# Kernel optimization log

Hardware: AMD Instinct MI355X
Metric: run time of the kernel (lower is better)

The kernel has to match this reference:

```python
import jax, jax.numpy as jnp
import numpy as np

H = 4  # n_heads in nn.MultiheadAttention
LN_EPS = 1e-5


def _mha_seq1(x_q, x_kv, in_w, in_b, out_w, out_b):
    """torch nn.MultiheadAttention with batch_first and seq_len=1 on q and kv.
    x_q, x_kv: [B, F]. in_w: [3F, F] (packed q/k/v), out_w: [F, F].
    With a single kv position, softmax over the kv axis is identically 1,
    so the output equals out_proj(v); we still compute scores/softmax so the
    math (and zero grads to Wq/Wk) matches torch exactly.
    """
    B, F = x_q.shape
    dh = F // H
    wq, wk, wv = jnp.split(in_w, 3, axis=0)
    bq, bk, bv = jnp.split(in_b, 3, axis=0)
    q = (x_q @ wq.T + bq).reshape(B, H, dh)
    k = (x_kv @ wk.T + bk).reshape(B, H, dh)
    v = (x_kv @ wv.T + bv).reshape(B, H, dh)
    s = jnp.einsum('bhd,bhd->bh', q, k) / jnp.sqrt(jnp.asarray(dh, x_q.dtype))
    w = jax.nn.softmax(s[..., None], axis=-1)  # [B, H, 1] == 1
    o = (w * v).reshape(B, F)
    return o @ out_w.T + out_b


def _layer_norm(x, g, b):
    mu = jnp.mean(x, axis=-1, keepdims=True)
    var = jnp.mean(jnp.square(x - mu), axis=-1, keepdims=True)
    return (x - mu) * jax.lax.rsqrt(var + LN_EPS) * g + b


def setup_inputs() -> dict:
    key = jax.random.key(0)
    B, GD, TD, F = 16384, 1024, 1024, 2048
    ks = jax.random.split(key, 20)
    s = 0.02  # weight init scale
    return {
        'graph_feat': jax.random.normal(ks[0], (B, GD), jnp.float32),
        'temporal_feat': jax.random.normal(ks[1], (B, TD), jnp.float32),
        'gp_w': jax.random.normal(ks[2], (F, GD), jnp.float32) * s,
        'gp_b': jax.random.normal(ks[3], (F,), jnp.float32) * s,
        'tp_w': jax.random.normal(ks[4], (F, TD), jnp.float32) * s,
        'tp_b': jax.random.normal(ks[5], (F,), jnp.float32) * s,
        'in1_w': jax.random.normal(ks[6], (3 * F, F), jnp.float32) * s,
        'in1_b': jax.random.normal(ks[7], (3 * F,), jnp.float32) * s,
        'out1_w': jax.random.normal(ks[8], (F, F), jnp.float32) * s,
        'out1_b': jax.random.normal(ks[9], (F,), jnp.float32) * s,
        'in2_w': jax.random.normal(ks[10], (3 * F, F), jnp.float32) * s,
        'in2_b': jax.random.normal(ks[11], (3 * F,), jnp.float32) * s,
        'out2_w': jax.random.normal(ks[12], (F, F), jnp.float32) * s,
        'out2_b': jax.random.normal(ks[13], (F,), jnp.float32) * s,
        'gate_w': jax.random.normal(ks[14], (F, 2 * F), jnp.float32) * s,
        'gate_b': jax.random.normal(ks[15], (F,), jnp.float32) * s,
        'ln_g': jnp.ones((F,), jnp.float32),
        'ln_b': jnp.zeros((F,), jnp.float32),
        'lin_w': jax.random.normal(ks[16], (F, F), jnp.float32) * s,
        'lin_b': jax.random.normal(ks[17], (F,), jnp.float32) * s,
    }


def reference(graph_feat, temporal_feat, gp_w, gp_b, tp_w, tp_b,
              in1_w, in1_b, out1_w, out1_b, in2_w, in2_b, out2_w, out2_b,
              gate_w, gate_b, ln_g, ln_b, lin_w, lin_b):
    g = graph_feat @ gp_w.T + gp_b          # [B, F]
    t = temporal_feat @ tp_w.T + tp_b       # [B, F]
    attn1 = _mha_seq1(g, t, in1_w, in1_b, out1_w, out1_b)  # cross1(g, t, t)
    attn2 = _mha_seq1(t, g, in2_w, in2_b, out2_w, out2_b)  # cross2(t, g, g)
    cross = attn1 + attn2
    gate = jax.nn.sigmoid(jnp.concatenate([g, cross], axis=-1) @ gate_w.T + gate_b)
    fused = gate * g + (1.0 - gate) * cross
    fused = _layer_norm(fused + g, ln_g, ln_b)
    return fused @ lin_w.T + lin_b
```

## Files before the change

kernel.cpp:

```cpp
#include <hip/hip_runtime.h>
#include <stdint.h>

typedef __attribute__((ext_vector_type(8))) short short8;
typedef __attribute__((ext_vector_type(4))) float f32x4;

__device__ __forceinline__ unsigned short f2bf(float f) {
  union { float f; uint32_t u; } v; v.f = f;
  uint32_t u = v.u;
  u += 0x7FFF + ((u >> 16) & 1);
  return (unsigned short)(u >> 16);
}
__device__ __forceinline__ float bf2f(unsigned short h) {
  union { uint32_t u; float f; } v; v.u = ((uint32_t)h) << 16;
  return v.f;
}

__global__ void conv_kernel(const float* __restrict__ in,
                            unsigned short* __restrict__ out, int n) {
  long i = ((long)blockIdx.x * blockDim.x + threadIdx.x) * 8;
  if (i >= n) return;
  float4 a = *(const float4*)(in + i);
  float4 b = *(const float4*)(in + i + 4);
  short8 s;
  s[0] = (short)f2bf(a.x); s[1] = (short)f2bf(a.y);
  s[2] = (short)f2bf(a.z); s[3] = (short)f2bf(a.w);
  s[4] = (short)f2bf(b.x); s[5] = (short)f2bf(b.y);
  s[6] = (short)f2bf(b.z); s[7] = (short)f2bf(b.w);
  *(short8*)(out + i) = s;
}

__global__ void convcat_kernel(const float* __restrict__ in,
                               unsigned short* __restrict__ out,
                               int colbase, int n) {
  long i = ((long)blockIdx.x * blockDim.x + threadIdx.x) * 8;
  if (i >= n) return;
  float4 a = *(const float4*)(in + i);
  float4 b = *(const float4*)(in + i + 4);
  short8 s;
  s[0] = (short)f2bf(a.x); s[1] = (short)f2bf(a.y);
  s[2] = (short)f2bf(a.z); s[3] = (short)f2bf(a.w);
  s[4] = (short)f2bf(b.x); s[5] = (short)f2bf(b.y);
  s[6] = (short)f2bf(b.z); s[7] = (short)f2bf(b.w);
  long row = i >> 10, col = i & 1023;
  *(short8*)(out + row * 2048 + colbase + col) = s;
}

__global__ void convs_kernel(const float* __restrict__ in,
                             const float* __restrict__ scale,
                             unsigned short* __restrict__ out, int n) {
  long i = ((long)blockIdx.x * blockDim.x + threadIdx.x) * 8;
  if (i >= n) return;
  short8 s;
#pragma unroll
  for (int j = 0; j < 8; ++j)
    s[j] = (short)f2bf(in[i + j] * scale[(i + j) & 2047]);
  *(short8*)(out + i) = s;
}

__global__ void tconv_kernel(const float* __restrict__ in, int R, int C,
                             unsigned short* __restrict__ out) {
  __shared__ float tile[32][33];
  int c0 = blockIdx.x * 32, r0 = blockIdx.y * 32;
  int tx = threadIdx.x, ty = threadIdx.y;
#pragma unroll
  for (int i = 0; i < 32; i += 8)
    tile[ty + i][tx] = in[(long)(r0 + ty + i) * C + c0 + tx];
  __syncthreads();
#pragma unroll
  for (int i = 0; i < 32; i += 8)
    out[(long)(c0 + ty + i) * R + r0 + tx] = f2bf(tile[tx][ty + i]);
}

enum { CE_PLAIN = 0, CE_WT = 1, CE_ACC = 2 };

template <int CE>
__global__ __launch_bounds__(256)
void compose_kernel(const unsigned short* __restrict__ A, int lda,
                    const unsigned short* __restrict__ W, int ldw,
                    unsigned short* C, int ldc,
                    unsigned short* Ct, long ctoff,
                    int K, int nmt,
                    int pairBase, long aoff, long woff, long coff) {
  constexpr int BK = 32;
  __shared__ unsigned short sA[128 * BK];
  __shared__ unsigned short sB[128 * BK];
  const int tid  = threadIdx.x;
  const int lane = tid & 63;
  const int wave = tid >> 6;
  const int wr = (wave >> 1) * 64;
  const int wc = (wave & 1) * 64;

  int bid = blockIdx.x;
  if (bid >= pairBase) {
    bid -= pairBase;
    A += aoff; W += woff; C += coff; Ct += ctoff;
  }
  const long tileM = (long)(bid % nmt) * 128;
  const long tileN = (long)(bid / nmt) * 128;

  const unsigned short* gA = A + (tileM + (tid >> 2)) * (long)lda + (tid & 3) * 8;
  const unsigned short* gB = W + (tileN + (tid >> 2)) * (long)ldw + (tid & 3) * 8;
  unsigned short* lA = sA + wave * 512;
  unsigned short* lB = sB + wave * 512;

  f32x4 acc[4][4] = {};
  const int fr = lane & 15;
  const int kb = (lane >> 4) * 8;

  for (int k0 = 0; k0 < K; k0 += BK) {
    __builtin_amdgcn_global_load_lds(
        (const __attribute__((address_space(1))) void*)(gA + k0),
        (__attribute__((address_space(3))) void*)(lA), 16, 0, 0);
    __builtin_amdgcn_global_load_lds(
        (const __attribute__((address_space(1))) void*)(gA + k0 + 64 * (long)lda),
        (__attribute__((address_space(3))) void*)(lA + 2048), 16, 0, 0);
    __builtin_amdgcn_global_load_lds(
        (const __attribute__((address_space(1))) void*)(gB + k0),
        (__attribute__((address_space(3))) void*)(lB), 16, 0, 0);
    __builtin_amdgcn_global_load_lds(
        (const __attribute__((address_space(1))) void*)(gB + k0 + 64 * (long)ldw),
        (__attribute__((address_space(3))) void*)(lB + 2048), 16, 0, 0);
    __syncthreads();

    short8 aF[4], bF[4];
#pragma unroll
    for (int m = 0; m < 4; ++m)
      aF[m] = *(const short8*)&sA[(wr + m * 16 + fr) * BK + kb];
#pragma unroll
    for (int n = 0; n < 4; ++n)
      bF[n] = *(const short8*)&sB[(wc + n * 16 + fr) * BK + kb];
#pragma unroll
    for (int m = 0; m < 4; ++m)
#pragma unroll
      for (int n = 0; n < 4; ++n)
        acc[m][n] = __builtin_amdgcn_mfma_f32_16x16x32_bf16(aF[m], bF[n], acc[m][n], 0, 0, 0);
    __syncthreads();
  }

  const int cr = (lane >> 4) * 4;
  const int cc = lane & 15;
#pragma unroll
  for (int m = 0; m < 4; ++m) {
    long r0 = tileM + wr + m * 16 + cr;
#pragma unroll
    for (int n = 0; n < 4; ++n) {
      long c = tileN + wc + n * 16 + cc;
#pragma unroll
      for (int r = 0; r < 4; ++r) {
        long idx = (r0 + r) * (long)ldc + c;
        float v = acc[m][n][r];
        if constexpr (CE == CE_ACC) v += bf2f(C[idx]);
        unsigned short bv = f2bf(v);
        C[idx] = bv;
        if constexpr (CE == CE_WT) Ct[c * 2048 + (r0 + r)] = bv;
      }
    }
  }
}

enum { EPI_BIAS = 0, EPI_GATE = 2, EPI_LNF32 = 4 };

#define VMW(N) asm volatile("s_waitcnt vmcnt(" #N ")" ::: "memory")
#define SBAR() __builtin_amdgcn_s_barrier()
#define SCB() __builtin_amdgcn_sched_barrier(0)

#define STG(D, OP, HALF, PTR, LD8)                                            \
  { char* lp_ = (char*)smem + ((D)*65536 + (OP)*32768 + (HALF)*16384 + w*2048); \
    __builtin_amdgcn_global_load_lds(                                         \
        (const __attribute__((address_space(1))) void*)(PTR),                 \
        (__attribute__((address_space(3))) void*)lp_, 16, 0, 0);              \
    __builtin_amdgcn_global_load_lds(                                         \
        (const __attribute__((address_space(1))) void*)((PTR) + (LD8)),       \
        (__attribute__((address_space(3))) void*)(lp_ + 1024), 16, 0, 0);     \
    (PTR) += 64; }
#define NOSTG ((void)0)

#define RDA(D, KK) ((KK) ? ((D) ? pA11 : pA01) : ((D) ? pA10 : pA00))
#define RDB(D, KK) ((KK) ? ((D) ? pB11 : pB01) : ((D) ? pB10 : pB00))

template <int EPI, int SWZ>
__global__ __launch_bounds__(512, 2)
void gemm8p_kernel(const unsigned short* __restrict__ A, int lda,
                   const unsigned short* __restrict__ W, int ldw,
                   int K, int ldc, int nmt,
                   const float* __restrict__ bias,
                   const float* __restrict__ bias2,
                   const unsigned short* Xg,
                   const unsigned short* Xc, int ldx,
                   const float2* __restrict__ stats,
                   void* Cv) {
  __shared__ unsigned short smem[65536];

  const int tid = threadIdx.x, lane = tid & 63, w = tid >> 6;
  const int wm = w >> 2, wn = w & 3;

  int bid = blockIdx.x;
  int mt, nt;
  if (SWZ) {
    const int xcd = bid & 7, seq = bid >> 3;
    nt = seq >> 3;
    mt = xcd * 8 + (seq & 7);
  } else {
    mt = bid % nmt;
    nt = bid / nmt;
  }
  const long tileM = (long)mt * 256, tileN = (long)nt * 256;

  const int sRow = w * 16 + (lane >> 3);
  const int sCol = (((lane & 7) ^ ((lane >> 3) & 7)) * 8);
  const unsigned short* pSA0 = A + (tileM + sRow) * (long)lda + sCol;
  const unsigned short* pSA1 = pSA0 + 128 * (long)lda;
  const unsigned short* pSB0 = W + (tileN + sRow) * (long)ldw + sCol;
  const unsigned short* pSB1 = pSB0 + 128 * (long)ldw;
  const long lda8 = 8 * (long)lda, ldw8 = 8 * (long)ldw;

  const int fr = lane & 15, kc = lane >> 4, l7 = lane & 7;
  const char* pA00 = (const char*)smem + (wm * 16 + fr) * 128 + ((kc) ^ l7) * 16;
  const char* pA01 = (const char*)smem + (wm * 16 + fr) * 128 + ((4 + kc) ^ l7) * 16;
  const char* pA10 = pA00 + 65536;
  const char* pA11 = pA01 + 65536;
  const char* pB00 = (const char*)smem + 32768 + (wn * 16 + fr) * 128 + ((kc) ^ l7) * 16;
  const char* pB01 = (const char*)smem + 32768 + (wn * 16 + fr) * 128 + ((4 + kc) ^ l7) * 16;
  const char* pB10 = pB00 + 65536;
  const char* pB11 = pB01 + 65536;

  f32x4 acc[8][4] = {};
  short8 aH[4][2];
  short8 bqS[2][2][2];

#define PHASE(D, MQ, NQ, LA, LB, STGX)                                        \
  {                                                                           \
    if (LA) {                                                                 \
      _Pragma("unroll") for (int mi = 0; mi < 4; ++mi) {                      \
        aH[mi][0] = *(const short8*)(RDA(D, 0) + (MQ)*16384 + mi * 4096);     \
        aH[mi][1] = *(const short8*)(RDA(D, 1) + (MQ)*16384 + mi * 4096);     \
      }                                                                       \
    }                                                                         \
    if (LB) {                                                                 \
      _Pragma("unroll") for (int ni = 0; ni < 2; ++ni) {                      \
        bqS[NQ][ni][0] = *(const short8*)(RDB(D, 0) + (NQ)*16384 + ni * 8192);\
        bqS[NQ][ni][1] = *(const short8*)(RDB(D, 1) + (NQ)*16384 + ni * 8192);\
      }                                                                       \
    }                                                                         \
    STGX;                                                                     \
    SCB();                                                                    \
    __builtin_amdgcn_s_setprio(1);                                            \
    _Pragma("unroll") for (int mi = 0; mi < 4; ++mi)                          \
    _Pragma("unroll") for (int ni = 0; ni < 2; ++ni) {                        \
      acc[(MQ)*4+mi][(NQ)*2+ni] = __builtin_amdgcn_mfma_f32_16x16x32_bf16(    \
          aH[mi][0], bqS[NQ][ni][0], acc[(MQ)*4+mi][(NQ)*2+ni], 0, 0, 0);     \
      acc[(MQ)*4+mi][(NQ)*2+ni] = __builtin_amdgcn_mfma_f32_16x16x32_bf16(    \
          aH[mi][1], bqS[NQ][ni][1], acc[(MQ)*4+mi][(NQ)*2+ni], 0, 0, 0);     \
    }                                                                         \
    __builtin_amdgcn_s_setprio(0);                                            \
    SCB();                                                                    \
  }

  STG(0, 0, 0, pSA0, lda8);
  STG(0, 1, 0, pSB0, ldw8);
  STG(0, 1, 1, pSB1, ldw8);
  STG(0, 0, 1, pSA1, lda8);
  STG(1, 0, 0, pSA0, lda8);
  STG(1, 1, 0, pSB0, ldw8);
  STG(1, 1, 1, pSB1, ldw8);
  STG(1, 0, 1, pSA1, lda8);
  VMW(12);
  SBAR();

  const int NIT = K / 128;
  for (int it = 0; it < NIT - 1; ++it) {
    PHASE(0, 0, 0, 1, 1, NOSTG);                               VMW(10); SBAR();
    PHASE(0, 0, 1, 0, 1, STG(0, 0, 0, pSA0, lda8);
                         STG(0, 1, 0, pSB0, ldw8));            VMW(12); SBAR();
    PHASE(0, 1, 0, 1, 0, STG(0, 1, 1, pSB1, ldw8));                     SBAR();
    PHASE(0, 1, 1, 0, 0, STG(0, 0, 1, pSA1, lda8));            VMW(12); SBAR();
    PHASE(1, 0, 0, 1, 1, NOSTG);                               VMW(10); SBAR();
    PHASE(1, 0, 1, 0, 1, STG(1, 0, 0, pSA0, lda8);
                         STG(1, 1, 0, pSB0, ldw8));            VMW(12); SBAR();
    PHASE(1, 1, 0, 1, 0, STG(1, 1, 1, pSB1, ldw8));                     SBAR();
    PHASE(1, 1, 1, 0, 0, STG(1, 0, 1, pSA1, lda8));            VMW(12); SBAR();
  }
  {
    PHASE(0, 0, 0, 1, 1, NOSTG); VMW(10); SBAR();
    PHASE(0, 0, 1, 0, 1, NOSTG); VMW(8);  SBAR();
    PHASE(0, 1, 0, 1, 0, NOSTG);          SBAR();
    PHASE(0, 1, 1, 0, 0, NOSTG); VMW(4);  SBAR();
    PHASE(1, 0, 0, 1, 1, NOSTG); VMW(2);  SBAR();
    PHASE(1, 0, 1, 0, 1, NOSTG); VMW(0);  SBAR();
    PHASE(1, 1, 0, 1, 0, NOSTG);          SBAR();
    PHASE(1, 1, 1, 0, 0, NOSTG);
  }
#undef PHASE

  const int cr = (lane >> 4) * 4;
  const int cc = lane & 15;
#pragma unroll
  for (int m = 0; m < 8; ++m) {
    long rr = tileM + (m >> 2) * 128 + (m & 3) * 32 + wm * 16 + cr;
#pragma unroll
    for (int n = 0; n < 4; ++n) {
      long c = tileN + (n >> 1) * 128 + (n & 1) * 64 + wn * 16 + cc;
      float b1 = bias ? bias[c] : 0.0f;
      float b2 = bias2 ? bias2[c] : 0.0f;
#pragma unroll
      for (int r = 0; r < 4; ++r) {
        long row = rr + r;
        long idx = row * (long)ldc + c;
        float v = acc[m][n][r];
        if constexpr (EPI == EPI_BIAS) {
          ((unsigned short*)Cv)[idx] = f2bf(v + b1 + b2);
        }
        if constexpr (EPI == EPI_GATE) {
          float gt = 1.0f / (1.0f + expf(-(v + b1)));
          long xix = row * (long)ldx + c;
          float gv = bf2f(Xg[xix]);
          float cvv = bf2f(Xc[xix]);
          ((unsigned short*)Cv)[idx] = f2bf(gt * gv + (1.0f - gt) * cvv + gv);
        }
        if constexpr (EPI == EPI_LNF32) {
          float2 st = stats[row];
          ((float*)Cv)[idx] = v * st.y - st.y * st.x * b1 + b2;
        }
      }
    }
  }
}

__global__ __launch_bounds__(256) void lnstats_kernel(
    const unsigned short* __restrict__ in, float2* __restrict__ stats) {
  const int row = blockIdx.x;
  const int t = threadIdx.x, lane = t & 63, wave = t >> 6;
  short8 v8 = *(const short8*)&in[(long)row * 2048 + t * 8];
  float s = 0.f, s2 = 0.f;
#pragma unroll
  for (int j = 0; j < 8; ++j) {
    float x = bf2f((unsigned short)v8[j]);
    s += x; s2 += x * x;
  }
#pragma unroll
  for (int off = 1; off < 64; off <<= 1) {
    s  += __shfl_xor(s, off);
    s2 += __shfl_xor(s2, off);
  }
  __shared__ float red[8];
  if (lane == 0) { red[wave] = s; red[4 + wave] = s2; }
  __syncthreads();
  if (t == 0) {
    float ts  = red[0] + red[1] + red[2] + red[3];
    float ts2 = red[4] + red[5] + red[6] + red[7];
    float mean = ts * (1.0f / 2048.0f);
    float var  = ts2 * (1.0f / 2048.0f) - mean * mean;
    stats[row] = make_float2(mean, rsqrtf(var + 1e-5f));
  }
}

__device__ __forceinline__ float blkRed(float s, float* red, int lane, int wave) {
#pragma unroll
  for (int off = 1; off < 64; off <<= 1) s += __shfl_xor(s, off);
  if (lane == 0) red[wave] = s;
  __syncthreads();
  return red[0] + red[1] + red[2] + red[3];
}

__global__ __launch_bounds__(256) void biascompP_kernel(
    const unsigned short* __restrict__ wO1b, const unsigned short* __restrict__ wO2b,
    const unsigned short* __restrict__ Wc1, const unsigned short* __restrict__ Wc2,
    const float* __restrict__ bv1, const float* __restrict__ bv2,
    const float* __restrict__ tpb, const float* __restrict__ gpb,
    const float* __restrict__ o1b, const float* __restrict__ o2b,
    float* __restrict__ bcV) {
  __shared__ float red[4];
  int c = blockIdx.x, t = threadIdx.x, lane = t & 63, wave = t >> 6;
  int k = t * 8;
  float s = 0.f;
  short8 a1 = *(const short8*)(wO1b + (long)c * 2048 + k);
  short8 a2 = *(const short8*)(wO2b + (long)c * 2048 + k);
  short8 a3 = *(const short8*)(Wc1 + (long)c * 2048 + k);
  short8 a4 = *(const short8*)(Wc2 + (long)c * 2048 + k);
#pragma unroll
  for (int j = 0; j < 8; ++j)
    s += bf2f((unsigned short)a1[j]) * bv1[k + j]
       + bf2f((unsigned short)a2[j]) * bv2[k + j]
       + bf2f((unsigned short)a3[j]) * tpb[k + j]
       + bf2f((unsigned short)a4[j]) * gpb[k + j];
  float tot = blkRed(s, red, lane, wave);
  if (t == 0) bcV[c] = tot + o1b[c] + o2b[c];
}

__global__ __launch_bounds__(256) void bgateP_kernel(
    const float* __restrict__ gate_w, const float* __restrict__ gate_b,
    const float* __restrict__ gpb, const float* __restrict__ bcV,
    float* __restrict__ bgateV) {
  __shared__ float red[4];
  int n = blockIdx.x, t = threadIdx.x, lane = t & 63, wave = t >> 6;
  const float* row = gate_w + (long)n * 4096;
  float s = 0.f;
  int k = t * 8;
#pragma unroll
  for (int j = 0; j < 8; ++j)
    s += row[k + j] * gpb[k + j] + row[2048 + k + j] * bcV[k + j];
  float tot = blkRed(s, red, lane, wave);
  if (t == 0) bgateV[n] = tot + gate_b[n];
}

__global__ __launch_bounds__(256) void uvP_kernel(
    const unsigned short* __restrict__ wlinp, const float* __restrict__ lin_w,
    const float* __restrict__ ln_beta, const float* __restrict__ lin_b,
    float* __restrict__ uV, float* __restrict__ vV) {
  __shared__ float redu[4], redv[4];
  int n = blockIdx.x, t = threadIdx.x, lane = t & 63, wave = t >> 6;
  int k = t * 8;
  short8 a1 = *(const short8*)(wlinp + (long)n * 2048 + k);
  float u = 0.f, v = 0.f;
#pragma unroll
  for (int j = 0; j < 8; ++j) {
    u += bf2f((unsigned short)a1[j]);
    v += ln_beta[k + j] * lin_w[(long)n * 2048 + k + j];
  }
#pragma unroll
  for (int off = 1; off < 64; off <<= 1) {
    u += __shfl_xor(u, off);
    v += __shfl_xor(v, off);
  }
  if (lane == 0) { redu[wave] = u; redv[wave] = v; }
  __syncthreads();
  if (t == 0) {
    uV[n] = redu[0] + redu[1] + redu[2] + redu[3];
    vV[n] = redv[0] + redv[1] + redv[2] + redv[3] + lin_b[n];
  }
}

extern "C" void kernel_launch(void* const* d_in, const int* in_sizes, int n_in,
                              void* d_out, int out_size, void* d_ws, size_t ws_size,
                              hipStream_t stream) {
  const float* graph    = (const float*)d_in[0];
  const float* temporal = (const float*)d_in[1];
  const float* gp_w  = (const float*)d_in[2];
  const float* gp_b  = (const float*)d_in[3];
  const float* tp_w  = (const float*)d_in[4];
  const float* tp_b  = (const float*)d_in[5];
  const float* in1_w = (const float*)d_in[6];
  const float* in1_b = (const float*)d_in[7];
  const float* out1_w = (const float*)d_in[8];
  const float* out1_b = (const float*)d_in[9];
  const float* in2_w = (const float*)d_in[10];
  const float* in2_b = (const float*)d_in[11];
  const float* out2_w = (const float*)d_in[12];
  const float* out2_b = (const float*)d_in[13];
  const float* gate_w = (const float*)d_in[14];
  const float* gate_b = (const float*)d_in[15];
  const float* ln_g  = (const float*)d_in[16];
  const float* ln_b  = (const float*)d_in[17];
  const float* lin_w = (const float*)d_in[18];
  const float* lin_b = (const float*)d_in[19];

  const int Bm = 16384, F = 2048, GD = 1024;
  const long BF = (long)Bm * F, FF = (long)F * F, FG = (long)F * GD;

  unsigned short* TG    = (unsigned short*)d_ws;
  unsigned short* Gbuf  = TG + BF;
  unsigned short* Cbuf  = Gbuf + BF;
  unsigned short* wLIN  = Cbuf + BF;
  float* bcV    = (float*)(wLIN + FF);
  float* bgateV = bcV + F;
  float* uV     = bgateV + F;
  float* vV     = uV + F;
  float2* stats = (float2*)(vV + F);

  unsigned short* DO      = (unsigned short*)d_out;
  unsigned short* wv1T    = DO;
  unsigned short* wv2T    = wv1T + FF;
  unsigned short* tpT     = wv2T + FF;
  unsigned short* gpT     = tpT + FG;
  unsigned short* Wc1     = gpT + FG;
  unsigned short* Wc2     = Wc1 + FF;
  unsigned short* wO1b    = Wc2 + FF;
  unsigned short* wO2b    = wO1b + FF;
  unsigned short* wGATEb  = wO2b + FF;
  unsigned short* wGP     = wGATEb + 2 * FF;
  unsigned short* Wcross  = wGP + FG;
  unsigned short* WcrossT = Wcross + FF;
  unsigned short* Wgate   = WcrossT + FF;

  auto conv = [&](const float* src, unsigned short* dst, long n) {
    conv_kernel<<<dim3((unsigned)(n / 8 / 256)), 256, 0, stream>>>(src, dst, (int)n);
  };
  convcat_kernel<<<dim3((unsigned)(Bm * GD / 8 / 256)), 256, 0, stream>>>(
      temporal, TG, 0, Bm * GD);
  convcat_kernel<<<dim3((unsigned)(Bm * GD / 8 / 256)), 256, 0, stream>>>(
      graph, TG, GD, Bm * GD);
  conv(gp_w, wGP, FG);
  conv(out1_w, wO1b, FF);
  conv(out2_w, wO2b, FF);
  conv(gate_w, wGATEb, 2 * FF);
  convs_kernel<<<dim3((unsigned)(FF / 8 / 256)), 256, 0, stream>>>(lin_w, ln_g, wLIN, (int)FF);
  tconv_kernel<<<dim3(F / 32, F / 32), dim3(32, 8), 0, stream>>>(in1_w + 2 * FF, F, F, wv1T);
  tconv_kernel<<<dim3(F / 32, F / 32), dim3(32, 8), 0, stream>>>(in2_w + 2 * FF, F, F, wv2T);
  tconv_kernel<<<dim3(GD / 32, F / 32), dim3(32, 8), 0, stream>>>(tp_w, F, GD, tpT);
  tconv_kernel<<<dim3(GD / 32, F / 32), dim3(32, 8), 0, stream>>>(gp_w, F, GD, gpT);

  compose_kernel<CE_PLAIN><<<dim3(512), dim3(256), 0, stream>>>(
      wO1b, F, wv1T, F, Wc1, F, nullptr, 0, F, 16,
      256, wO2b - wO1b, wv2T - wv1T, Wc2 - Wc1);
  compose_kernel<CE_WT><<<dim3(256), dim3(256), 0, stream>>>(
      Wc1, F, tpT, F, Wcross, F, WcrossT, (long)1024 * 2048, F, 16,
      128, Wc2 - Wc1, gpT - tpT, 1024);
  biascompP_kernel<<<dim3(F), dim3(256), 0, stream>>>(
      wO1b, wO2b, Wc1, Wc2, in1_b + 2 * F, in2_b + 2 * F, tp_b, gp_b,
      out1_b, out2_b, bcV);
  compose_kernel<CE_PLAIN><<<dim3(256), dim3(256), 0, stream>>>(
      wGATEb + F, 2 * F, WcrossT, F, Wgate, F, nullptr, 0, F, 16,
      1 << 30, 0, 0, 0);
  compose_kernel<CE_ACC><<<dim3(128), dim3(256), 0, stream>>>(
      wGATEb, 2 * F, gpT, F, Wgate + GD, F, nullptr, 0, F, 16,
      1 << 30, 0, 0, 0);
  bgateP_kernel<<<dim3(F), dim3(256), 0, stream>>>(gate_w, gate_b, gp_b, bcV, bgateV);
  uvP_kernel<<<dim3(F), dim3(256), 0, stream>>>(wLIN, lin_w, ln_b, lin_b, uV, vV);

  dim3 blk(512), grid(512);
  gemm8p_kernel<EPI_BIAS, 1><<<grid, blk, 0, stream>>>(
      TG + GD, F, wGP, GD, GD, F, 0,
      gp_b, nullptr, nullptr, nullptr, 0, nullptr, Gbuf);
  gemm8p_kernel<EPI_BIAS, 1><<<grid, blk, 0, stream>>>(
      TG, F, Wcross, F, F, F, 0,
      bcV, nullptr, nullptr, nullptr, 0, nullptr, Cbuf);
  gemm8p_kernel<EPI_GATE, 1><<<grid, blk, 0, stream>>>(
      TG, F, Wgate, F, F, F, 0,
      bgateV, nullptr, Gbuf, Cbuf, F, nullptr, Gbuf);
  lnstats_kernel<<<dim3(Bm), dim3(256), 0, stream>>>(Gbuf, stats);
  gemm8p_kernel<EPI_LNF32, 1><<<grid, blk, 0, stream>>>(
      Gbuf, F, wLIN, F, F, F, 0,
      uV, vV, nullptr, nullptr, 0, stats, (void*)d_out);
}
```

Baseline: 892.4 us.

## Merge cross and gate GEMMs into one wide GEMM and fuse gating into stats kernel

The cross and gate GEMMs share the same A operand (TG), so their weights are now stacked into one [2F x F] matrix and computed in a single GEMM with N=4096 and a concatenated bias. The sigmoid gating, residual add and LayerNorm statistics move out of the GEMM epilogue into one row-wise kernel that reads the cross and logit halves plus G, writes the fused bf16 result and computes mean and rstd. This drops one kernel launch and the separate re-read of Cbuf in the gate epilogue, at the cost of an extra bf16 round trip of the logits through memory. The buffers are reorganised so the output buffer serves as scratch for the combined GEMM result.

```diff
diff --git a/kernel.cpp b/kernel.cpp
--- a/kernel.cpp
+++ b/kernel.cpp
@@ -158,7 +158,7 @@
   }
 }
 
-enum { EPI_BIAS = 0, EPI_GATE = 2, EPI_LNF32 = 4 };
+enum { EPI_BIAS = 0, EPI_LNF32 = 4 };
 
 #define VMW(N) asm volatile("s_waitcnt vmcnt(" #N ")" ::: "memory")
 #define SBAR() __builtin_amdgcn_s_barrier()
@@ -185,8 +185,6 @@
                    int K, int ldc, int nmt,
                    const float* __restrict__ bias,
                    const float* __restrict__ bias2,
-                   const unsigned short* Xg,
-                   const unsigned short* Xc, int ldx,
                    const float2* __restrict__ stats,
                    void* Cv) {
   __shared__ unsigned short smem[65536];
@@ -310,13 +308,6 @@
         if constexpr (EPI == EPI_BIAS) {
           ((unsigned short*)Cv)[idx] = f2bf(v + b1 + b2);
         }
-        if constexpr (EPI == EPI_GATE) {
-          float gt = 1.0f / (1.0f + expf(-(v + b1)));
-          long xix = row * (long)ldx + c;
-          float gv = bf2f(Xg[xix]);
-          float cvv = bf2f(Xc[xix]);
-          ((unsigned short*)Cv)[idx] = f2bf(gt * gv + (1.0f - gt) * cvv + gv);
-        }
         if constexpr (EPI == EPI_LNF32) {
           float2 st = stats[row];
           ((float*)Cv)[idx] = v * st.y - st.y * st.x * b1 + b2;
@@ -326,17 +317,28 @@
   }
 }
 
-__global__ __launch_bounds__(256) void lnstats_kernel(
-    const unsigned short* __restrict__ in, float2* __restrict__ stats) {
+__global__ __launch_bounds__(256) void fusestats_kernel(
+    const unsigned short* __restrict__ CL, const unsigned short* __restrict__ G,
+    unsigned short* __restrict__ PL, float2* __restrict__ stats) {
   const int row = blockIdx.x;
   const int t = threadIdx.x, lane = t & 63, wave = t >> 6;
-  short8 v8 = *(const short8*)&in[(long)row * 2048 + t * 8];
+  short8 xc = *(const short8*)&CL[(long)row * 4096 + t * 8];
+  short8 xl = *(const short8*)&CL[(long)row * 4096 + 2048 + t * 8];
+  short8 xg = *(const short8*)&G[(long)row * 2048 + t * 8];
+  short8 o8;
   float s = 0.f, s2 = 0.f;
 #pragma unroll
   for (int j = 0; j < 8; ++j) {
-    float x = bf2f((unsigned short)v8[j]);
+    float cv = bf2f((unsigned short)xc[j]);
+    float lv = bf2f((unsigned short)xl[j]);
+    float gv = bf2f((unsigned short)xg[j]);
+    float gt = 1.0f / (1.0f + expf(-lv));
+    unsigned short pb = f2bf(gt * gv + (1.0f - gt) * cv + gv);
+    o8[j] = (short)pb;
+    float x = bf2f(pb);
     s += x; s2 += x * x;
   }
+  *(short8*)(PL + (long)row * 2048 + t * 8) = o8;
 #pragma unroll
   for (int off = 1; off < 64; off <<= 1) {
     s  += __shfl_xor(s, off);
@@ -457,13 +459,16 @@
   const int Bm = 16384, F = 2048, GD = 1024;
   const long BF = (long)Bm * F, FF = (long)F * F, FG = (long)F * GD;
 
-  unsigned short* TG    = (unsigned short*)d_ws;
-  unsigned short* Gbuf  = TG + BF;
-  unsigned short* Cbuf  = Gbuf + BF;
-  unsigned short* wLIN  = Cbuf + BF;
-  float* bcV    = (float*)(wLIN + FF);
-  float* bgateV = bcV + F;
-  float* uV     = bgateV + F;
+  unsigned short* TG   = (unsigned short*)d_ws;
+  unsigned short* PL   = TG;
+  unsigned short* Gbuf = TG + BF;
+  unsigned short* wLIN = Gbuf + BF;
+  unsigned short* wGP  = wLIN + FF;
+  unsigned short* Wcg  = wGP + FG;
+  unsigned short* Wcross = Wcg;
+  unsigned short* Wgate  = Wcg + FF;
+  float* bc2V   = (float*)(Wcg + 2 * FF);
+  float* uV     = bc2V + 2 * F;
   float* vV     = uV + F;
   float2* stats = (float2*)(vV + F);
 
@@ -477,10 +482,8 @@
   unsigned short* wO1b    = Wc2 + FF;
   unsigned short* wO2b    = wO1b + FF;
   unsigned short* wGATEb  = wO2b + FF;
-  unsigned short* wGP     = wGATEb + 2 * FF;
-  unsigned short* Wcross  = wGP + FG;
-  unsigned short* WcrossT = Wcross + FF;
-  unsigned short* Wgate   = WcrossT + FF;
+  unsigned short* WcrossT = wGATEb + 2 * FF;
+  unsigned short* CL      = DO;
 
   auto conv = [&](const float* src, unsigned short* dst, long n) {
     conv_kernel<<<dim3((unsigned)(n / 8 / 256)), 256, 0, stream>>>(src, dst, (int)n);
@@ -507,28 +510,26 @@
       128, Wc2 - Wc1, gpT - tpT, 1024);
   biascompP_kernel<<<dim3(F), dim3(256), 0, stream>>>(
       wO1b, wO2b, Wc1, Wc2, in1_b + 2 * F, in2_b + 2 * F, tp_b, gp_b,
-      out1_b, out2_b, bcV);
+      out1_b, out2_b, bc2V);
   compose_kernel<CE_PLAIN><<<dim3(256), dim3(256), 0, stream>>>(
       wGATEb + F, 2 * F, WcrossT, F, Wgate, F, nullptr, 0, F, 16,
       1 << 30, 0, 0, 0);
   compose_kernel<CE_ACC><<<dim3(128), dim3(256), 0, stream>>>(
       wGATEb, 2 * F, gpT, F, Wgate + GD, F, nullptr, 0, F, 16,
       1 << 30, 0, 0, 0);
-  bgateP_kernel<<<dim3(F), dim3(256), 0, stream>>>(gate_w, gate_b, gp_b, bcV, bgateV);
+  bgateP_kernel<<<dim3(F), dim3(256), 0, stream>>>(gate_w, gate_b, gp_b, bc2V,
+                                                   bc2V + F);
   uvP_kernel<<<dim3(F), dim3(256), 0, stream>>>(wLIN, lin_w, ln_b, lin_b, uV, vV);
 
-  dim3 blk(512), grid(512);
-  gemm8p_kernel<EPI_BIAS, 1><<<grid, blk, 0, stream>>>(
+  dim3 blk(512);
+  gemm8p_kernel<EPI_BIAS, 1><<<dim3(512), blk, 0, stream>>>(
       TG + GD, F, wGP, GD, GD, F, 0,
-      gp_b, nullptr, nullptr, nullptr, 0, nullptr, Gbuf);
-  gemm8p_kernel<EPI_BIAS, 1><<<grid, blk, 0, stream>>>(
-      TG, F, Wcross, F, F, F, 0,
-      bcV, nullptr, nullptr, nullptr, 0, nullptr, Cbuf);
-  gemm8p_kernel<EPI_GATE, 1><<<grid, blk, 0, stream>>>(
-      TG, F, Wgate, F, F, F, 0,
-      bgateV, nullptr, Gbuf, Cbuf, F, nullptr, Gbuf);
-  lnstats_kernel<<<dim3(Bm), dim3(256), 0, stream>>>(Gbuf, stats);
-  gemm8p_kernel<EPI_LNF32, 1><<<grid, blk, 0, stream>>>(
-      Gbuf, F, wLIN, F, F, F, 0,
-      uV, vV, nullptr, nullptr, 0, stats, (void*)d_out);
-}
+      gp_b, nullptr, nullptr, Gbuf);
+  gemm8p_kernel<EPI_BIAS, 1><<<dim3(1024), blk, 0, stream>>>(
+      TG, F, Wcg, F, F, 2 * F, 0,
+      bc2V, nullptr, nullptr, CL);
+  fusestats_kernel<<<dim3(Bm), dim3(256), 0, stream>>>(CL, Gbuf, PL, stats);
+  gemm8p_kernel<EPI_LNF32, 1><<<dim3(512), blk, 0, stream>>>(
+      PL, F, wLIN, F, F, F, 0,
+      uV, vV, stats, (void*)d_out);
+}
```

Measured after the change: 806.9 us. 1.11x faster.
